# Optimization experiments

Hardware: AMD Instinct MI355X
Metric: run time of the kernel (lower is better)

Reference implementation:

```python
import jax, jax.numpy as jnp
import numpy as np
from jax import lax


def setup_inputs() -> dict:
    key = jax.random.key(0)
    ks = jax.random.split(key, 8)
    B, L, H = 2, 1024, 2048
    E = 2
    d = H * E            # d_inner = 4096
    S = 16               # state_dim
    R = 128              # dt_rank = ceil(H / 16)
    sc = lambda fan_in: 1.0 / np.sqrt(fan_in)
    return {
        "x": jax.random.normal(ks[0], (B, L, H), jnp.float32),
        "W_in": jax.random.normal(ks[1], (H, 2 * d), jnp.float32) * sc(H),
        "conv_w": jax.random.normal(ks[2], (d, 1, 3), jnp.float32) * sc(3),
        "conv_b": jnp.zeros((d,), jnp.float32),
        "W_x": jax.random.normal(ks[3], (d, R + 2 * S), jnp.float32) * sc(d),
        "W_dt": jax.random.normal(ks[4], (R, d), jnp.float32) * sc(R),
        "b_dt": jnp.zeros((d,), jnp.float32),
        "A_log": jnp.log(jnp.tile(jnp.arange(1, S + 1, dtype=jnp.float32), (d, 1))),
        "D": jnp.ones((d,), jnp.float32),
        "W_out": jax.random.normal(ks[5], (d, H), jnp.float32) * sc(d),
    }


def reference(x, W_in, conv_w, conv_b, W_x, W_dt, b_dt, A_log, D, W_out):
    d = conv_b.shape[0]
    S = A_log.shape[1]
    R = W_dt.shape[0]
    # in_proj and gate split
    xz = x @ W_in                              # [B, L, 2d]
    xp, z = jnp.split(xz, 2, axis=-1)          # each [B, L, d]
    # depthwise conv1d (kernel 3, pad 1)
    xc = lax.conv_general_dilated(
        jnp.transpose(xp, (0, 2, 1)), conv_w, (1,), [(1, 1)],
        feature_group_count=d, dimension_numbers=("NCH", "OIH", "NCH"))
    xc = jnp.transpose(xc + conv_b[None, :, None], (0, 2, 1))  # [B, L, d]
    xc = jax.nn.silu(xc)
    # x_proj -> dt, B, C
    x_dbl = xc @ W_x                           # [B, L, R + 2S]
    dt_in = x_dbl[..., :R]
    Bm = x_dbl[..., R:R + S]                   # [B, L, S]
    Cm = x_dbl[..., R + S:]                    # [B, L, S]
    dt = jax.nn.softplus(dt_in @ W_dt + b_dt)  # [B, L, d]
    A = -jnp.exp(A_log)                        # [d, S]

    def step(h, ins):
        u_t, dt_t, B_t, C_t = ins              # [B,d], [B,d], [B,S], [B,S]
        dA = jnp.exp(dt_t[:, :, None] * A)     # [B, d, S]
        h = dA * h + dt_t[:, :, None] * B_t[:, None, :] * u_t[:, :, None]
        y_t = jnp.einsum("bds,bs->bd", h, C_t)
        return h, y_t

    h0 = jnp.zeros((x.shape[0], d, S), xc.dtype)
    xsT = (jnp.swapaxes(xc, 0, 1), jnp.swapaxes(dt, 0, 1),
           jnp.swapaxes(Bm, 0, 1), jnp.swapaxes(Cm, 0, 1))
    _, yT = lax.scan(step, h0, xsT)            # yT: [L, B, d]
    y = jnp.swapaxes(yT, 0, 1) + xc * D        # skip connection
    y = y * jax.nn.silu(z)                     # gate
    return y @ W_out                           # [B, L, H]
```

## Files before the change

kernel.cpp:

```cpp
#include <hip/hip_runtime.h>
#include <hip/hip_bf16.h>


using u16 = unsigned short;
typedef __bf16 bf16x8 __attribute__((ext_vector_type(8)));
typedef float f32x4 __attribute__((ext_vector_type(4)));
typedef u16 u16x8 __attribute__((ext_vector_type(8)));

#define NCHUNK 16
#define CLEN   64
#define SWZ(row, q) ((q) ^ (((row) >> 1) & 3))

__device__ __forceinline__ float bf2f(u16 u) {
    union { unsigned int i; float f; } v; v.i = ((unsigned int)u) << 16; return v.f;
}
__device__ __forceinline__ u16 f2bf(float f) {
    union { float f; unsigned int i; } v; v.f = f;
    unsigned int x = v.i;
    return (u16)((x + 0x7FFFu + ((x >> 16) & 1u)) >> 16);
}

__device__ __forceinline__ float* hloc_ptr(u16* xzbase, int i) {
    return reinterpret_cast<float*>(xzbase + (size_t)(i >> 11) * 8192) + (i & 2047);
}
__device__ __forceinline__ float* hin_ptr(u16* xzbase, int i) {
    return reinterpret_cast<float*>(xzbase + (size_t)((i >> 11) + 1024) * 8192) + (i & 2047);
}

__global__ void detect_dtype(const u16* __restrict__ xraw, int* __restrict__ flag) {
    __shared__ int cnt[256];
    const int tid = threadIdx.x;
    int plausible = 0;
    for (int i = tid; i < 4096; i += 256) {
        const u16 v = xraw[2 * i];
        const int e = (v >> 7) & 0xFF;
        plausible += (e >= 100 && e <= 145) ? 1 : 0;
    }
    cnt[tid] = plausible;
    __syncthreads();
    for (int s = 128; s > 0; s >>= 1) {
        if (tid < s) cnt[tid] += cnt[tid + s];
        __syncthreads();
    }
    if (tid == 0) *flag = (cnt[0] > 2458) ? 1 : 0;
}

__device__ __forceinline__ void cvt_seg8(const void* src, u16* dst, int i8,
                                         bool isbf) {
    if (isbf) {
        *(u16x8*)&dst[i8 * 8] = *((const u16x8*)src + i8);
    } else {
        const float* f = (const float*)src + i8 * 8;
        u16x8 o;
#pragma unroll
        for (int j = 0; j < 8; j++) o[j] = f2bf(f[j]);
        *(u16x8*)&dst[i8 * 8] = o;
    }
}
__global__ void cvt_fused(const void* __restrict__ x_raw, u16* __restrict__ xcan,
                          const void* __restrict__ cw_raw, u16* __restrict__ cw_c,
                          const void* __restrict__ cb_raw, u16* __restrict__ cb_c,
                          const void* __restrict__ bdt_raw, u16* __restrict__ bdt_c,
                          const void* __restrict__ Alog_raw, u16* __restrict__ Alog_c,
                          const void* __restrict__ D_raw, u16* __restrict__ D_c,
                          const int* __restrict__ flag) {
    const bool isbf = (*flag != 0);
    int blk = blockIdx.x;
    const int tid = threadIdx.x;
    if (blk < 2048) { cvt_seg8(x_raw, xcan, blk * 256 + tid, isbf); return; }
    blk -= 2048;
    if (blk < 6)  { cvt_seg8(cw_raw, cw_c, blk * 256 + tid, isbf); return; }
    blk -= 6;
    if (blk < 2)  { cvt_seg8(cb_raw, cb_c, blk * 256 + tid, isbf); return; }
    blk -= 2;
    if (blk < 2)  { cvt_seg8(bdt_raw, bdt_c, blk * 256 + tid, isbf); return; }
    blk -= 2;
    if (blk < 32) { cvt_seg8(Alog_raw, Alog_c, blk * 256 + tid, isbf); return; }
    blk -= 32;
    cvt_seg8(D_raw, D_c, blk * 256 + tid, isbf);
}

__device__ __forceinline__ void tr_tile(const void* in, u16* out, int R, int C,
                                        int bx, int by, int tx, int ty, bool isbf,
                                        u16 (*tile)[34]) {
    const int c0 = bx * 32, r0 = by * 64;
    const int cp = tx & 15, rh = tx >> 4;
#pragma unroll
    for (int i = 0; i < 4; i++) {
        const int row = ty + rh * 8 + i * 16;
        const size_t idx = (size_t)(r0 + row) * C + c0 + cp * 2;
        if (isbf) {
            union { unsigned int u; u16 h[2]; } p;
            p.u = *reinterpret_cast<const unsigned int*>(&((const u16*)in)[idx]);
            tile[row][cp * 2] = p.h[0];
            tile[row][cp * 2 + 1] = p.h[1];
        } else {
            const float2 f = *reinterpret_cast<const float2*>(&((const float*)in)[idx]);
            tile[row][cp * 2] = f2bf(f.x);
            tile[row][cp * 2 + 1] = f2bf(f.y);
        }
    }
    __syncthreads();
#pragma unroll
    for (int i = 0; i < 4; i++) {
        const int w = ty + i * 8;
        union { u16 h[2]; unsigned int u; } p;
        p.h[0] = tile[2 * tx][w];
        p.h[1] = tile[2 * tx + 1][w];
        *reinterpret_cast<unsigned int*>(&out[(size_t)(c0 + w) * R + r0 + 2 * tx]) = p.u;
    }
}
__global__ void transpose_fused(const void* __restrict__ Wi, u16* __restrict__ WiT,
                                const void* __restrict__ Wo, u16* __restrict__ WoT,
                                const void* __restrict__ Wd, u16* __restrict__ WdT,
                                const void* __restrict__ Wx, u16* __restrict__ WxT,
                                const int* __restrict__ flag) {
    __shared__ u16 tile[64][34];
    const bool isbf = (*flag != 0);
    const int tx = threadIdx.x, ty = threadIdx.y;
    int blk = blockIdx.x;
    if (blk < 8192) { tr_tile(Wi, WiT, 2048, 8192, blk % 256, blk / 256, tx, ty, isbf, tile); return; }
    blk -= 8192;
    if (blk < 4096) { tr_tile(Wo, WoT, 4096, 2048, blk % 64, blk / 64, tx, ty, isbf, tile); return; }
    blk -= 4096;
    if (blk < 256)  { tr_tile(Wd, WdT, 128, 4096, blk % 128, blk / 128, tx, ty, isbf, tile); return; }
    blk -= 256;
    tr_tile(Wx, WxT, 4096, 160, blk % 5, blk / 5, tx, ty, isbf, tile);
}

template <int BM, int BN, int THR>
__device__ __forceinline__ void stage_ring(const u16* __restrict__ Ab,
                                           const u16* __restrict__ Bb,
                                           int K, int k0, u16* dst, int tid)
{
    constexpr int CHA = BM * 4, CHB = BN * 4;
    static_assert(CHA % THR == 0 && CHB % THR == 0, "chunk/thread mismatch");
#pragma unroll
    for (int it = 0; it < CHA / THR; it++) {
        const int c = it * THR + tid;
        const int row = c >> 2, kc = SWZ(row, c & 3);
        __builtin_amdgcn_global_load_lds(
            (const __attribute__((address_space(1))) void*)(Ab + (size_t)row * K + k0 + kc * 8),
            (__attribute__((address_space(3))) void*)(dst + c * 8), 16, 0, 0);
    }
#pragma unroll
    for (int it = 0; it < CHB / THR; it++) {
        const int c = it * THR + tid;
        const int row = c >> 2, kc = SWZ(row, c & 3);
        __builtin_amdgcn_global_load_lds(
            (const __attribute__((address_space(1))) void*)(Bb + (size_t)row * K + k0 + kc * 8),
            (__attribute__((address_space(3))) void*)(dst + BM * 32 + c * 8), 16, 0, 0);
    }
}

template <int BM, int BN, int WM, int WN, int MODE>
__global__ __launch_bounds__(64 * WM * WN, 2) void gemm_ring(
    const u16* __restrict__ A, const u16* __restrict__ Bt, void* __restrict__ C,
    const int* __restrict__ oflagp, int M, int N, int K)
{
    constexpr int THR = 64 * WM * WN;
    constexpr int MT  = BM / (WM * 16);
    constexpr int NT  = BN / (WN * 16);
    constexpr int NPH = 2;
    constexpr int GM  = MT / NPH;
    constexpr int STG = (BM + BN) * 32;
    static_assert((BM * 4 + BN * 4) / THR == 4, "vmcnt ladder assumes 4 loads/thread/stage");
    static_assert(MT % NPH == 0, "MT must split into NPH phases");
    extern __shared__ u16 smem[];

    const int tid  = threadIdx.x;
    const int lane = tid & 63;
    const int wave = tid >> 6;
    const int wm = wave / WN, wn = wave % WN;
    const int q  = lane >> 4;
    const int n0 = blockIdx.x * BN;
    const int m0 = blockIdx.y * BM;
    const int NTILE = K >> 5;

    const u16* Ab = A  + (size_t)m0 * K;
    const u16* Bb = Bt + (size_t)n0 * K;

    stage_ring<BM, BN, THR>(Ab, Bb, K, 0,  smem + 0 * STG, tid);
    stage_ring<BM, BN, THR>(Ab, Bb, K, 32, smem + 1 * STG, tid);
    stage_ring<BM, BN, THR>(Ab, Bb, K, 64, smem + 2 * STG, tid);

    f32x4 acc[MT][NT];
#pragma unroll
    for (int mi = 0; mi < MT; mi++)
#pragma unroll
        for (int ni = 0; ni < NT; ni++)
            acc[mi][ni] = (f32x4){0.f, 0.f, 0.f, 0.f};

    const int arow = wm * (MT * 16) + (lane & 15);
    const int brow = wn * (NT * 16) + (lane & 15);

    for (int t = 0; t < NTILE; t++) {
        const int tp = t + 3;
        if (tp < NTILE) {
            stage_ring<BM, BN, THR>(Ab, Bb, K, tp * 32, smem + (tp & 3) * STG, tid);
            asm volatile("s_waitcnt vmcnt(12)" ::: "memory");
        } else if (tp == NTILE) {
            asm volatile("s_waitcnt vmcnt(8)" ::: "memory");
        } else if (tp == NTILE + 1) {
            asm volatile("s_waitcnt vmcnt(4)" ::: "memory");
        } else {
            asm volatile("s_waitcnt vmcnt(0)" ::: "memory");
        }
        __builtin_amdgcn_s_barrier();

        const u16* As = smem + (t & 3) * STG;
        const u16* Bs = As + BM * 32;
        bf16x8 bfr[NT];
#pragma unroll
        for (int ni = 0; ni < NT; ni++) {
            const int r = brow + ni * 16;
            bfr[ni] = *reinterpret_cast<const bf16x8*>(&Bs[r * 32 + SWZ(r, q) * 8]);
        }
#pragma unroll
        for (int g = 0; g < NPH; g++) {
            bf16x8 af[GM];
#pragma unroll
            for (int i = 0; i < GM; i++) {
                const int r = arow + (g * GM + i) * 16;
                af[i] = *reinterpret_cast<const bf16x8*>(&As[r * 32 + SWZ(r, q) * 8]);
            }
            __builtin_amdgcn_s_setprio(1);
#pragma unroll
            for (int i = 0; i < GM; i++)
#pragma unroll
                for (int ni = 0; ni < NT; ni++)
                    acc[g * GM + i][ni] = __builtin_amdgcn_mfma_f32_16x16x32_bf16(
                        af[i], bfr[ni], acc[g * GM + i][ni], 0, 0, 0);
            __builtin_amdgcn_s_setprio(0);
            __builtin_amdgcn_sched_barrier(0);
            __builtin_amdgcn_s_barrier();
        }
    }

    int oflag = 1;
    if constexpr (MODE == 1) oflag = *oflagp;

    const int rb = m0 + wm * (MT * 16) + (q << 2);
    const int cb = n0 + wn * (NT * 16) + (lane & 15);
#pragma unroll
    for (int mi = 0; mi < MT; mi++) {
#pragma unroll
        for (int ni = 0; ni < NT; ni++) {
            const int col = cb + ni * 16;
#pragma unroll
            for (int r = 0; r < 4; r++) {
                const int row = rb + mi * 16 + r;
                const float v = acc[mi][ni][r];
                if constexpr (MODE == 0) {
                    ((u16*)C)[(size_t)row * N + col] = f2bf(v);
                } else {
                    if (oflag) ((u16*)C)[(size_t)row * N + col] = f2bf(v);
                    else       ((float*)C)[(size_t)row * N + col] = v;
                }
            }
        }
    }
}

template <int BM, int BN, int BK, int WR, int WC, int MT, int NT, int MODE>
__global__ __launch_bounds__(256) void gemm_bt(
    const u16* __restrict__ A, const u16* __restrict__ Bt,
    void* __restrict__ C, const u16* __restrict__ bias,
    const int* __restrict__ oflagp,
    int M, int N, int K)
{
    static_assert(BK == 32, "BK=32 (one 16x16x32 MFMA k-slab)");
    __shared__ u16 As[BM * BK];
    __shared__ u16 Bs[BN * BK];

    const int tid  = threadIdx.x;
    const int lane = tid & 63;
    const int wave = tid >> 6;
    const int wm = wave / WC, wn = wave % WC;

    const int m0 = blockIdx.y * BM;
    const int n0 = blockIdx.x * BN;
    const int Kchunk = K / gridDim.z;
    const int kbeg = blockIdx.z * Kchunk;
    const int kend = kbeg + Kchunk;

    f32x4 acc[MT][NT];
#pragma unroll
    for (int mi = 0; mi < MT; mi++)
#pragma unroll
        for (int ni = 0; ni < NT; ni++)
            acc[mi][ni] = (f32x4){0.f, 0.f, 0.f, 0.f};

    const int q = lane >> 4;
    const int arow = wm * MT * 16 + (lane & 15);
    const int brow = wn * NT * 16 + (lane & 15);

    constexpr int CHA = BM * 4;
    constexpr int CHB = BN * 4;

    for (int k0 = kbeg; k0 < kend; k0 += BK) {
        __syncthreads();
#pragma unroll
        for (int it = 0; it < (CHA + 255) / 256; it++) {
            const int c = it * 256 + tid;
            if (CHA % 256 == 0 || c < CHA) {
                const int row = c >> 2, kc = SWZ(row, c & 3);
                const u16* gp = &A[(size_t)(m0 + row) * K + k0 + kc * 8];
                __builtin_amdgcn_global_load_lds(
                    (const __attribute__((address_space(1))) void*)gp,
                    (__attribute__((address_space(3))) void*)&As[c * 8], 16, 0, 0);
            }
        }
#pragma unroll
        for (int it = 0; it < (CHB + 255) / 256; it++) {
            const int c = it * 256 + tid;
            if (CHB % 256 == 0 || c < CHB) {
                const int row = c >> 2, kc = SWZ(row, c & 3);
                const u16* gp = &Bt[(size_t)(n0 + row) * K + k0 + kc * 8];
                __builtin_amdgcn_global_load_lds(
                    (const __attribute__((address_space(1))) void*)gp,
                    (__attribute__((address_space(3))) void*)&Bs[c * 8], 16, 0, 0);
            }
        }
        __syncthreads();

        bf16x8 af[MT], bfr[NT];
#pragma unroll
        for (int mi = 0; mi < MT; mi++) {
            const int row = arow + mi * 16;
            af[mi] = *reinterpret_cast<const bf16x8*>(&As[row * BK + SWZ(row, q) * 8]);
        }
#pragma unroll
        for (int ni = 0; ni < NT; ni++) {
            const int row = brow + ni * 16;
            bfr[ni] = *reinterpret_cast<const bf16x8*>(&Bs[row * BK + SWZ(row, q) * 8]);
        }
#pragma unroll
        for (int mi = 0; mi < MT; mi++)
#pragma unroll
            for (int ni = 0; ni < NT; ni++)
                acc[mi][ni] = __builtin_amdgcn_mfma_f32_16x16x32_bf16(
                    af[mi], bfr[ni], acc[mi][ni], 0, 0, 0);
    }

    const int rb = m0 + wm * MT * 16 + ((lane >> 4) << 2);
    const int cb = n0 + wn * NT * 16 + (lane & 15);
#pragma unroll
    for (int mi = 0; mi < MT; mi++) {
#pragma unroll
        for (int ni = 0; ni < NT; ni++) {
            const int col = cb + ni * 16;
#pragma unroll
            for (int r = 0; r < 4; r++) {
                const int row = rb + mi * 16 + r;
                const float v = acc[mi][ni][r];
                if constexpr (MODE == 0) {
                    ((u16*)C)[(size_t)row * N + col] = f2bf(v);
                } else if constexpr (MODE == 5) {
                    ((float*)C)[((size_t)blockIdx.z * M + row) * N + col] = v;
                }
            }
        }
    }
}

__global__ void reduce_xdbl(const float* __restrict__ part,
                            float* __restrict__ x_dbl, u16* __restrict__ dtin) {
    const int idx = blockIdx.x * 256 + threadIdx.x;
    const int row = idx / 160, col = idx - row * 160;
    float s = 0.f;
#pragma unroll
    for (int z = 0; z < 8; z++) s += part[(size_t)z * (2048 * 160) + idx];
    x_dbl[idx] = s;
    if (col < 128) dtin[row * 128 + col] = f2bf(s);
}

__global__ __launch_bounds__(256) void dt_gemm(
    const u16* __restrict__ A,
    const u16* __restrict__ Bt,
    float* __restrict__ C,
    const u16* __restrict__ bias)
{
    __shared__ ulong4 smem_raw[2048];
    u16* As = (u16*)smem_raw;
    u16* Bs = As + 64 * 128;
    float* Cs = (float*)smem_raw;

    const int tid  = threadIdx.x;
    const int lane = tid & 63;
    const int wave = tid >> 6;
    const int n0 = blockIdx.x * 64;
    const int m0 = blockIdx.y * 64;

#pragma unroll
    for (int it = 0; it < 4; it++) {
        const int c = it * 256 + tid;
        const int row = c >> 4, cc = (c & 15) ^ (row & 7);
        const u16* gp = &A[(size_t)(m0 + row) * 128 + cc * 8];
        __builtin_amdgcn_global_load_lds(
            (const __attribute__((address_space(1))) void*)gp,
            (__attribute__((address_space(3))) void*)&As[c * 8], 16, 0, 0);
    }
#pragma unroll
    for (int it = 0; it < 4; it++) {
        const int c = it * 256 + tid;
        const int row = c >> 4, cc = (c & 15) ^ (row & 7);
        const u16* gp = &Bt[(size_t)(n0 + row) * 128 + cc * 8];
        __builtin_amdgcn_global_load_lds(
            (const __attribute__((address_space(1))) void*)gp,
            (__attribute__((address_space(3))) void*)&Bs[c * 8], 16, 0, 0);
    }
    __syncthreads();

    const int q  = lane >> 4;
    const int ar = wave * 16 + (lane & 15);
    f32x4 acc[4];
#pragma unroll
    for (int ni = 0; ni < 4; ni++) acc[ni] = (f32x4){0.f, 0.f, 0.f, 0.f};

#pragma unroll
    for (int kk = 0; kk < 4; kk++) {
        const int cA = kk * 4 + q;
        const bf16x8 af = *reinterpret_cast<const bf16x8*>(
            &As[(ar * 16 + (cA ^ (ar & 7))) * 8]);
#pragma unroll
        for (int ni = 0; ni < 4; ni++) {
            const int br = ni * 16 + (lane & 15);
            const bf16x8 bfr = *reinterpret_cast<const bf16x8*>(
                &Bs[(br * 16 + (cA ^ (br & 7))) * 8]);
            acc[ni] = __builtin_amdgcn_mfma_f32_16x16x32_bf16(af, bfr, acc[ni], 0, 0, 0);
        }
    }
    __syncthreads();

#pragma unroll
    for (int ni = 0; ni < 4; ni++) {
        const int col = ni * 16 + (lane & 15);
#pragma unroll
        for (int r = 0; r < 4; r++) {
            const int rowl = wave * 16 + q * 4 + r;
            Cs[rowl * 68 + col] = acc[ni][r];
        }
    }
    __syncthreads();

#pragma unroll
    for (int p = 0; p < 4; p++) {
        const int rowl = p * 16 + (tid >> 4);
        const int c0 = (tid & 15) * 4;
        float4 v = *reinterpret_cast<const float4*>(&Cs[rowl * 68 + c0]);
        float* vp = reinterpret_cast<float*>(&v);
#pragma unroll
        for (int j = 0; j < 4; j++) {
            const float x = vp[j] + bf2f(bias[n0 + c0 + j]);
            vp[j] = fmaxf(x, 0.f) + __logf(1.f + __expf(-fabsf(x)));
        }
        *reinterpret_cast<float4*>(&C[(size_t)(m0 + rowl) * 4096 + n0 + c0]) = v;
    }
}

__global__ void conv_silu(const u16* __restrict__ xz, const u16* __restrict__ conv_w,
                          const u16* __restrict__ conv_b, u16* __restrict__ xc) {
    const int idx = blockIdx.x * 256 + threadIdx.x;
    const int row = idx >> 9, c0 = (idx & 511) * 8;
    const int l = row & 1023;

    u16 wcat[24];
    *(u16x8*)&wcat[0]  = *(const u16x8*)&conv_w[c0 * 3];
    *(u16x8*)&wcat[8]  = *(const u16x8*)&conv_w[c0 * 3 + 8];
    *(u16x8*)&wcat[16] = *(const u16x8*)&conv_w[c0 * 3 + 16];
    const u16x8 bv = *(const u16x8*)&conv_b[c0];
    const u16x8 x0 = *(const u16x8*)&xz[(size_t)row * 8192 + c0];
    u16x8 xm = {}, xp = {};
    if (l > 0)    xm = *(const u16x8*)&xz[(size_t)(row - 1) * 8192 + c0];
    if (l < 1023) xp = *(const u16x8*)&xz[(size_t)(row + 1) * 8192 + c0];

    u16x8 out;
#pragma unroll
    for (int i = 0; i < 8; i++) {
        float v = bf2f(wcat[3 * i]) * bf2f(xm[i])
                + bf2f(wcat[3 * i + 1]) * bf2f(x0[i])
                + bf2f(wcat[3 * i + 2]) * bf2f(xp[i])
                + bf2f(bv[i]);
        v = v / (1.f + __expf(-v));
        out[i] = f2bf(v);
    }
    *(u16x8*)&xc[(size_t)row * 4096 + c0] = out;
}

__global__ __launch_bounds__(256) void scan_p1(
    const float* __restrict__ dt, const u16* __restrict__ xc,
    const float* __restrict__ x_dbl, const u16* __restrict__ A_log,
    float* __restrict__ Parr, u16* __restrict__ xzbase)
{
    __shared__ float Bsm[CLEN][16];
    const int tid = threadIdx.x;
    const int nc = blockIdx.x, cg = blockIdx.y, b = blockIdx.z;
    const int ch = cg * 256 + tid;
    const size_t row0 = (size_t)b * 1024 + nc * CLEN;

    {
        const int t = tid >> 2, q = tid & 3;
        const float4 v = *(const float4*)&x_dbl[(row0 + t) * 160 + 128 + q * 4];
        *(float4*)&Bsm[t][q * 4] = v;
    }
    __syncthreads();

    float A_s[16], h[16];
#pragma unroll
    for (int s = 0; s < 16; s++) {
        A_s[s] = -__expf(bf2f(A_log[ch * 16 + s]));
        h[s] = 0.f;
    }
    float Sdt = 0.f;

    float dt_v = dt[row0 * 4096 + ch];
    float u_v  = bf2f(xc[row0 * 4096 + ch]);
    for (int t = 0; t < CLEN; t++) {
        const int tn = (t + 1 < CLEN) ? t + 1 : t;
        const float dt_n = dt[(row0 + tn) * 4096 + ch];
        const float u_n  = bf2f(xc[(row0 + tn) * 4096 + ch]);
        const float dtu = dt_v * u_v;
        Sdt += dt_v;
        const f32x4* Brow = (const f32x4*)&Bsm[t][0];
        const f32x4 B0 = Brow[0], B1 = Brow[1], B2 = Brow[2], B3 = Brow[3];
#pragma unroll
        for (int s = 0; s < 16; s++) {
            const float Bs_ = (s < 4 ? B0[s & 3] : s < 8 ? B1[s & 3] : s < 12 ? B2[s & 3] : B3[s & 3]);
            const float dA = __expf(dt_v * A_s[s]);
            h[s] = dA * h[s] + dtu * Bs_;
        }
        dt_v = dt_n; u_v = u_n;
    }
    const int i0 = (((b * NCHUNK + nc) * 4096) + ch) * 16;
    float* pp = &Parr[i0];
    float* hp = hloc_ptr(xzbase, i0);
#pragma unroll
    for (int s4 = 0; s4 < 4; s4++) {
        float4 pq, hq;
        pq.x = __expf(A_s[4 * s4 + 0] * Sdt);
        pq.y = __expf(A_s[4 * s4 + 1] * Sdt);
        pq.z = __expf(A_s[4 * s4 + 2] * Sdt);
        pq.w = __expf(A_s[4 * s4 + 3] * Sdt);
        hq.x = h[4 * s4 + 0]; hq.y = h[4 * s4 + 1];
        hq.z = h[4 * s4 + 2]; hq.w = h[4 * s4 + 3];
        *(float4*)&pp[4 * s4] = pq;
        *(float4*)&hp[4 * s4] = hq;
    }
}

__global__ __launch_bounds__(256) void scan_p2(
    const float* __restrict__ Parr, u16* __restrict__ xzbase)
{
    const int tid = threadIdx.x;
    const int lane = tid & 63, wave = tid >> 6;
    const int blk = blockIdx.x;
    const int b = blk >> 8, cg = blk & 255;
    const int c_local = lane & 3, s = lane >> 2;
    const int ch = cg * 16 + wave * 4 + c_local;

    float Pv[NCHUNK], hl[NCHUNK];
#pragma unroll
    for (int c = 0; c < NCHUNK; c++) {
        const int i = (((b * NCHUNK + c) * 4096) + ch) * 16 + s;
        Pv[c] = Parr[i];
        hl[c] = *hloc_ptr(xzbase, i);
    }
    float hin = 0.f;
#pragma unroll
    for (int c = 0; c < NCHUNK; c++) {
        const int i = (((b * NCHUNK + c) * 4096) + ch) * 16 + s;
        *hin_ptr(xzbase, i) = hin;
        hin = Pv[c] * hin + hl[c];
    }
}

__global__ __launch_bounds__(256) void scan_p3(
    const float* __restrict__ dt, const u16* __restrict__ xc,
    const float* __restrict__ x_dbl, const u16* __restrict__ xz,
    const u16* __restrict__ A_log, const u16* __restrict__ Dp,
    u16* __restrict__ yg, u16* __restrict__ xzbase)
{
    __shared__ float BCs[CLEN][32];
    const int tid = threadIdx.x;
    const int nc = blockIdx.x, cg = blockIdx.y, b = blockIdx.z;
    const int ch = cg * 256 + tid;
    const size_t row0 = (size_t)b * 1024 + nc * CLEN;

#pragma unroll
    for (int it = 0; it < 2; it++) {
        const int c = it * 256 + tid;
        const int t = c >> 3, q = c & 7;
        const float4 v = *(const float4*)&x_dbl[(row0 + t) * 160 + 128 + q * 4];
        *(float4*)&BCs[t][q * 4] = v;
    }
    __syncthreads();

    float A_s[16], h[16];
    const int i0 = (((b * NCHUNK + nc) * 4096) + ch) * 16;
    {
        const float* hp = hin_ptr(xzbase, i0);
#pragma unroll
        for (int s4 = 0; s4 < 4; s4++) {
            const float4 hq = *(const float4*)&hp[4 * s4];
            h[4 * s4 + 0] = hq.x; h[4 * s4 + 1] = hq.y;
            h[4 * s4 + 2] = hq.z; h[4 * s4 + 3] = hq.w;
        }
    }
#pragma unroll
    for (int s = 0; s < 16; s++)
        A_s[s] = -__expf(bf2f(A_log[ch * 16 + s]));
    const float D_ch = bf2f(Dp[ch]);

    float dt_v = dt[row0 * 4096 + ch];
    float u_v  = bf2f(xc[row0 * 4096 + ch]);
    float z_v  = bf2f(xz[row0 * 8192 + 4096 + ch]);
    for (int t = 0; t < CLEN; t++) {
        const int tn = (t + 1 < CLEN) ? t + 1 : t;
        const size_t rn = row0 + tn;
        const float dt_n = dt[rn * 4096 + ch];
        const float u_n  = bf2f(xc[rn * 4096 + ch]);
        const float z_n  = bf2f(xz[rn * 8192 + 4096 + ch]);
        const float dtu = dt_v * u_v;

        const f32x4* Row = (const f32x4*)&BCs[t][0];
        const f32x4 B0 = Row[0], B1 = Row[1], B2 = Row[2], B3 = Row[3];
        const f32x4 C0 = Row[4], C1 = Row[5], C2 = Row[6], C3 = Row[7];

        float y0 = 0.f, y1 = 0.f, y2 = 0.f, y3 = 0.f;
#pragma unroll
        for (int s = 0; s < 16; s++) {
            const float Bs_ = (s < 4 ? B0[s & 3] : s < 8 ? B1[s & 3] : s < 12 ? B2[s & 3] : B3[s & 3]);
            const float Cs_ = (s < 4 ? C0[s & 3] : s < 8 ? C1[s & 3] : s < 12 ? C2[s & 3] : C3[s & 3]);
            const float dA = __expf(dt_v * A_s[s]);
            h[s] = dA * h[s] + dtu * Bs_;
            const float hc = h[s] * Cs_;
            if ((s & 3) == 0) y0 += hc; else if ((s & 3) == 1) y1 += hc;
            else if ((s & 3) == 2) y2 += hc; else y3 += hc;
        }
        const float y = (y0 + y1) + (y2 + y3);
        const float silu_z = z_v / (1.f + __expf(-z_v));
        yg[(row0 + t) * 4096 + ch] = f2bf((y + u_v * D_ch) * silu_z);
        dt_v = dt_n; u_v = u_n; z_v = z_n;
    }
}

extern "C" void kernel_launch(void* const* d_in, const int* in_sizes, int n_in,
                              void* d_out, int out_size, void* d_ws, size_t ws_size,
                              hipStream_t stream)
{
    const void* x_raw      = d_in[0];
    const void* W_in_raw   = d_in[1];
    const void* conv_w_raw = d_in[2];
    const void* conv_b_raw = d_in[3];
    const void* W_x_raw    = d_in[4];
    const void* W_dt_raw   = d_in[5];
    const void* b_dt_raw   = d_in[6];
    const void* A_log_raw  = d_in[7];
    const void* D_raw      = d_in[8];
    const void* W_out_raw  = d_in[9];

    char* ws = (char*)d_ws;
    size_t off = 0;
    auto alloc = [&](size_t bytes) { char* p = ws + off; off += (bytes + 255) & ~(size_t)255; return p; };
    int*   flag   = (int*)  alloc(4);
    u16*   W_inT  = (u16*)  alloc(8192ULL * 2048 * 2);
    u16*   W_outT = (u16*)  alloc(2048ULL * 4096 * 2);
    u16*   W_dtT  = (u16*)  alloc(4096ULL * 128 * 2);
    u16*   W_xT   = (u16*)  alloc(160ULL * 4096 * 2);
    u16*   xz     = (u16*)  alloc(2048ULL * 8192 * 2);
    u16*   xc     = (u16*)  alloc(2048ULL * 4096 * 2);
    float* x_dbl  = (float*)alloc(2048ULL * 160 * 4);
    u16*   dtin   = (u16*)  alloc(2048ULL * 128 * 2);
    u16*   yg     = (u16*)  alloc(2048ULL * 4096 * 2);
    u16*   xcan   = (u16*)  alloc(2048ULL * 2048 * 2);
    float* xdblp  = (float*)alloc(8ULL * 2048 * 160 * 4);
    u16*   cw_c   = (u16*)  alloc(12288 * 2);
    u16*   cb_c   = (u16*)  alloc(4096 * 2);
    u16*   bdt_c  = (u16*)  alloc(4096 * 2);
    u16*   Alog_c = (u16*)  alloc(65536 * 2);
    u16*   D_c    = (u16*)  alloc(4096 * 2);
    float* dtv    = (float*)W_inT;
    float* Parr   = (float*)xcan;

    detect_dtype<<<1, 256, 0, stream>>>((const u16*)x_raw, flag);
    cvt_fused<<<2048 + 6 + 2 + 2 + 32 + 2, 256, 0, stream>>>(
        x_raw, xcan, conv_w_raw, cw_c, conv_b_raw, cb_c, b_dt_raw, bdt_c,
        A_log_raw, Alog_c, D_raw, D_c, flag);

    transpose_fused<<<8192 + 4096 + 256 + 320, dim3(32, 8), 0, stream>>>(
        W_in_raw, W_inT, W_out_raw, W_outT, W_dt_raw, W_dtT, W_x_raw, W_xT, flag);

    (void)hipFuncSetAttribute(
        reinterpret_cast<const void*>(&gemm_ring<256, 256, 2, 4, 0>),
        hipFuncAttributeMaxDynamicSharedMemorySize, 131072);
    gemm_ring<256, 256, 2, 4, 0><<<dim3(8192 / 256, 2048 / 256), 512, 131072, stream>>>(
        xcan, W_inT, xz, nullptr, 2048, 8192, 2048);

    conv_silu<<<(2048 * 512) / 256, 256, 0, stream>>>(xz, cw_c, cb_c, xc);

    gemm_bt<64, 160, 32, 4, 1, 1, 10, 5>
        <<<dim3(1, 2048 / 64, 8), 256, 0, stream>>>(xc, W_xT, xdblp, nullptr, nullptr, 2048, 160, 4096);

    reduce_xdbl<<<(2048 * 160) / 256, 256, 0, stream>>>(xdblp, x_dbl, dtin);

    dt_gemm<<<dim3(4096 / 64, 2048 / 64), 256, 0, stream>>>(dtin, W_dtT, dtv, bdt_c);

    scan_p1<<<dim3(NCHUNK, 16, 2), 256, 0, stream>>>(dtv, xc, x_dbl, Alog_c, Parr, xz);
    scan_p2<<<512, 256, 0, stream>>>(Parr, xz);
    scan_p3<<<dim3(NCHUNK, 16, 2), 256, 0, stream>>>(dtv, xc, x_dbl, xz, Alog_c, D_c, yg, xz);

    (void)hipFuncSetAttribute(
        reinterpret_cast<const void*>(&gemm_ring<128, 128, 2, 2, 1>),
        hipFuncAttributeMaxDynamicSharedMemorySize, 65536);
    gemm_ring<128, 128, 2, 2, 1><<<dim3(2048 / 128, 2048 / 128), 256, 65536, stream>>>(
        yg, W_outT, d_out, flag, 2048, 2048, 4096);
}
```

Before: 408.8 us.

## Split-K the output projection GEMM and prefetch next A-fragment phase

The output projection GEMM (2048x2048x4096) now uses split-K with two K halves across gridDim.z, writing fp32 partials into a reused scratch buffer, followed by a new reduce_out kernel that sums them and converts to the output dtype. This doubles the block count from 256 so the GPU's compute units are better filled. Separately, the ring GEMM now loads the next phase's A fragments before issuing the current phase's MFMAs, to overlap LDS reads with matrix math. The cost is extra fp32 partial traffic, one more kernel launch, and higher register pressure from holding all A fragments.

```diff
diff --git a/kernel.cpp b/kernel.cpp
--- a/kernel.cpp
+++ b/kernel.cpp
@@ -6,6 +6,7 @@
 typedef __bf16 bf16x8 __attribute__((ext_vector_type(8)));
 typedef float f32x4 __attribute__((ext_vector_type(4)));
 typedef u16 u16x8 __attribute__((ext_vector_type(8)));
+typedef u16 u16x4 __attribute__((ext_vector_type(4)));
 
 #define NCHUNK 16
 #define CLEN   64
@@ -175,10 +176,12 @@
     const int q  = lane >> 4;
     const int n0 = blockIdx.x * BN;
     const int m0 = blockIdx.y * BM;
-    const int NTILE = K >> 5;
-
-    const u16* Ab = A  + (size_t)m0 * K;
-    const u16* Bb = Bt + (size_t)n0 * K;
+    const int Kchunk = K / gridDim.z;
+    const int kbeg = blockIdx.z * Kchunk;
+    const int NTILE = Kchunk >> 5;
+
+    const u16* Ab = A  + (size_t)m0 * K + kbeg;
+    const u16* Bb = Bt + (size_t)n0 * K + kbeg;
 
     stage_ring<BM, BN, THR>(Ab, Bb, K, 0,  smem + 0 * STG, tid);
     stage_ring<BM, BN, THR>(Ab, Bb, K, 32, smem + 1 * STG, tid);
@@ -210,19 +213,26 @@
 
         const u16* As = smem + (t & 3) * STG;
         const u16* Bs = As + BM * 32;
-        bf16x8 bfr[NT];
+        bf16x8 bfr[NT], af[MT];
 #pragma unroll
         for (int ni = 0; ni < NT; ni++) {
             const int r = brow + ni * 16;
             bfr[ni] = *reinterpret_cast<const bf16x8*>(&Bs[r * 32 + SWZ(r, q) * 8]);
         }
 #pragma unroll
+        for (int i = 0; i < GM; i++) {
+            const int r = arow + i * 16;
+            af[i] = *reinterpret_cast<const bf16x8*>(&As[r * 32 + SWZ(r, q) * 8]);
+        }
+#pragma unroll
         for (int g = 0; g < NPH; g++) {
-            bf16x8 af[GM];
-#pragma unroll
-            for (int i = 0; i < GM; i++) {
-                const int r = arow + (g * GM + i) * 16;
-                af[i] = *reinterpret_cast<const bf16x8*>(&As[r * 32 + SWZ(r, q) * 8]);
+            if (g + 1 < NPH) {
+#pragma unroll
+                for (int i = 0; i < GM; i++) {
+                    const int r = arow + ((g + 1) * GM + i) * 16;
+                    af[(g + 1) * GM + i] =
+                        *reinterpret_cast<const bf16x8*>(&As[r * 32 + SWZ(r, q) * 8]);
+                }
             }
             __builtin_amdgcn_s_setprio(1);
 #pragma unroll
@@ -230,7 +240,7 @@
 #pragma unroll
                 for (int ni = 0; ni < NT; ni++)
                     acc[g * GM + i][ni] = __builtin_amdgcn_mfma_f32_16x16x32_bf16(
-                        af[i], bfr[ni], acc[g * GM + i][ni], 0, 0, 0);
+                        af[g * GM + i], bfr[ni], acc[g * GM + i][ni], 0, 0, 0);
             __builtin_amdgcn_s_setprio(0);
             __builtin_amdgcn_sched_barrier(0);
             __builtin_amdgcn_s_barrier();
@@ -253,12 +263,31 @@
                 const float v = acc[mi][ni][r];
                 if constexpr (MODE == 0) {
                     ((u16*)C)[(size_t)row * N + col] = f2bf(v);
+                } else if constexpr (MODE == 2) {
+                    ((float*)C)[((size_t)blockIdx.z * M + row) * N + col] = v;
                 } else {
                     if (oflag) ((u16*)C)[(size_t)row * N + col] = f2bf(v);
                     else       ((float*)C)[(size_t)row * N + col] = v;
                 }
             }
         }
+    }
+}
+
+__global__ void reduce_out(const float* __restrict__ part, void* __restrict__ out,
+                           const int* __restrict__ flag) {
+    const int idx = blockIdx.x * 256 + threadIdx.x;
+    const int i4 = idx * 4;
+    const float4 a = *(const float4*)&part[i4];
+    const float4 b = *(const float4*)&part[(size_t)4194304 + i4];
+    if (*flag) {
+        u16x4 o;
+        o[0] = f2bf(a.x + b.x); o[1] = f2bf(a.y + b.y);
+        o[2] = f2bf(a.z + b.z); o[3] = f2bf(a.w + b.w);
+        *(u16x4*)&((u16*)out)[i4] = o;
+    } else {
+        float4 s = {a.x + b.x, a.y + b.y, a.z + b.z, a.w + b.w};
+        *(float4*)&((float*)out)[i4] = s;
     }
 }
 
@@ -682,6 +711,7 @@
     u16*   D_c    = (u16*)  alloc(4096 * 2);
     float* dtv    = (float*)W_inT;
     float* Parr   = (float*)xcan;
+    float* outp   = (float*)W_inT;
 
     detect_dtype<<<1, 256, 0, stream>>>((const u16*)x_raw, flag);
     cvt_fused<<<2048 + 6 + 2 + 2 + 32 + 2, 256, 0, stream>>>(
@@ -694,7 +724,7 @@
     (void)hipFuncSetAttribute(
         reinterpret_cast<const void*>(&gemm_ring<256, 256, 2, 4, 0>),
         hipFuncAttributeMaxDynamicSharedMemorySize, 131072);
-    gemm_ring<256, 256, 2, 4, 0><<<dim3(8192 / 256, 2048 / 256), 512, 131072, stream>>>(
+    gemm_ring<256, 256, 2, 4, 0><<<dim3(8192 / 256, 2048 / 256, 1), 512, 131072, stream>>>(
         xcan, W_inT, xz, nullptr, 2048, 8192, 2048);
 
     conv_silu<<<(2048 * 512) / 256, 256, 0, stream>>>(xz, cw_c, cb_c, xc);
@@ -711,8 +741,9 @@
     scan_p3<<<dim3(NCHUNK, 16, 2), 256, 0, stream>>>(dtv, xc, x_dbl, xz, Alog_c, D_c, yg, xz);
 
     (void)hipFuncSetAttribute(
-        reinterpret_cast<const void*>(&gemm_ring<128, 128, 2, 2, 1>),
+        reinterpret_cast<const void*>(&gemm_ring<128, 128, 2, 2, 2>),
         hipFuncAttributeMaxDynamicSharedMemorySize, 65536);
-    gemm_ring<128, 128, 2, 2, 1><<<dim3(2048 / 128, 2048 / 128), 256, 65536, stream>>>(
-        yg, W_outT, d_out, flag, 2048, 2048, 4096);
-}
+    gemm_ring<128, 128, 2, 2, 2><<<dim3(2048 / 128, 2048 / 128, 2), 256, 65536, stream>>>(
+        yg, W_outT, outp, nullptr, 2048, 2048, 4096);
+    reduce_out<<<(2048 * 2048 / 4) / 256, 256, 0, stream>>>(outp, d_out, flag);
+}
```

Result: no change. 407.3 us (-0.4%).
